# Kernel optimization log

Measured on AMD Instinct MI355X. Metric: run time of the kernel, lower is better.

The kernel has to match this reference:

```python
import math
import jax, jax.numpy as jnp
import numpy as np

D_MODEL = 1024
NUM_HEADS = 16
HEAD_DIM = D_MODEL // NUM_HEADS
CAUSAL = True


def setup_inputs() -> dict:
    key = jax.random.key(0)
    ks = jax.random.split(key, 9)
    B, S = 2, 2048
    s = 1.0 / math.sqrt(D_MODEL)
    x = jax.random.normal(ks[0], (B, S, D_MODEL), dtype=jnp.float32)
    Wq = jax.random.normal(ks[1], (D_MODEL, D_MODEL), dtype=jnp.float32) * s
    bq = jax.random.normal(ks[2], (D_MODEL,), dtype=jnp.float32) * 0.01
    Wk = jax.random.normal(ks[3], (D_MODEL, D_MODEL), dtype=jnp.float32) * s
    bk = jax.random.normal(ks[4], (D_MODEL,), dtype=jnp.float32) * 0.01
    Wv = jax.random.normal(ks[5], (D_MODEL, D_MODEL), dtype=jnp.float32) * s
    bv = jax.random.normal(ks[6], (D_MODEL,), dtype=jnp.float32) * 0.01
    Wo = jax.random.normal(ks[7], (D_MODEL, D_MODEL), dtype=jnp.float32) * s
    bo = jax.random.normal(ks[8], (D_MODEL,), dtype=jnp.float32) * 0.01
    return {"x": x, "Wq": Wq, "bq": bq, "Wk": Wk, "bk": bk,
            "Wv": Wv, "bv": bv, "Wo": Wo, "bo": bo}


def reference(x, Wq, bq, Wk, bk, Wv, bv, Wo, bo):
    B, S, _ = x.shape
    # projections (torch Linear: x @ W.T + b; here W already stored as [in,out])
    q = x @ Wq + bq
    k = x @ Wk + bk
    v = x @ Wv + bv
    # split heads -> [B, H, S, hd]
    def split(t):
        return t.reshape(B, S, NUM_HEADS, HEAD_DIM).transpose(0, 2, 1, 3)
    q, k, v = split(q), split(k), split(v)
    scores = jnp.einsum('bhqd,bhkd->bhqk', q, k) / math.sqrt(HEAD_DIM)
    if CAUSAL:
        causal = jnp.tril(jnp.ones((S, S), dtype=bool))  # True = keep
        scores = jnp.where(causal, scores, -jnp.inf)
    attn = jax.nn.softmax(scores, axis=-1)
    out = jnp.einsum('bhqk,bhkd->bhqd', attn, v)
    out = out.transpose(0, 2, 1, 3).reshape(B, S, D_MODEL)
    return out @ Wo + bo
```

## Files before the change

### kernel.cpp

```cpp
#include <hip/hip_runtime.h>
#include <hip/hip_bf16.h>

typedef __bf16 bf16_t;
typedef __bf16 v8bf __attribute__((ext_vector_type(8)));
typedef float  v4f  __attribute__((ext_vector_type(4)));

#define MFMA16(a, b, c) __builtin_amdgcn_mfma_f32_16x16x32_bf16((a), (b), (c), 0, 0, 0)

#define GLDS16(g, l) __builtin_amdgcn_global_load_lds(                         \
    (const __attribute__((address_space(1))) void*)(g),                        \
    (__attribute__((address_space(3))) void*)(l), 16, 0, 0)

#define VMEMCNT(n) asm volatile("s_waitcnt vmcnt(" #n ")" ::: "memory")
#define SBAR()     __builtin_amdgcn_s_barrier()
#define SFENCE()   __builtin_amdgcn_sched_barrier(0)

#define B_SZ   2
#define SEQ    2048
#define DM     1024
#define NH     16
#define HD     64
#define M_TOT  4096

#define QSCALE 0.18033688011112043f

__global__ __launch_bounds__(256)
void conv_x_kernel(const float* __restrict__ src, bf16_t* __restrict__ dst)
{
    int i = (blockIdx.x * 256 + threadIdx.x) * 8;
    float4 a = *reinterpret_cast<const float4*>(src + i);
    float4 b = *reinterpret_cast<const float4*>(src + i + 4);
    union { bf16_t h[8]; int4 v; } u;
    u.h[0] = (bf16_t)a.x; u.h[1] = (bf16_t)a.y; u.h[2] = (bf16_t)a.z; u.h[3] = (bf16_t)a.w;
    u.h[4] = (bf16_t)b.x; u.h[5] = (bf16_t)b.y; u.h[6] = (bf16_t)b.z; u.h[7] = (bf16_t)b.w;
    *reinterpret_cast<int4*>(dst + i) = u.v;
}

__global__ __launch_bounds__(256)
void conv_wt_kernel(const float* __restrict__ Wq, const float* __restrict__ Wk,
                    const float* __restrict__ Wv, const float* __restrict__ Wo,
                    bf16_t* __restrict__ WqkvT, bf16_t* __restrict__ WoT)
{
    __shared__ float t[32][33];
    const int z = blockIdx.z;
    const float* src = (z == 0) ? Wq : (z == 1) ? Wk : (z == 2) ? Wv : Wo;
    bf16_t* dst = (z < 3) ? (WqkvT + (size_t)z * 1048576) : WoT;
    const int tx = threadIdx.x & 31, ty = threadIdx.x >> 5;
    const int c0 = blockIdx.x * 32, r0 = blockIdx.y * 32;
#pragma unroll
    for (int i = 0; i < 4; ++i)
        t[ty + i * 8][tx] = src[(size_t)(r0 + ty + i * 8) * DM + c0 + tx];
    __syncthreads();
#pragma unroll
    for (int i = 0; i < 4; ++i)
        dst[(size_t)(c0 + ty + i * 8) * DM + r0 + tx] = (bf16_t)t[tx][ty + i * 8];
}

__global__ __launch_bounds__(256)
void gemm_qkv_kernel(const bf16_t* __restrict__ A, const bf16_t* __restrict__ BT,
                     const float* __restrict__ b0, const float* __restrict__ b1,
                     const float* __restrict__ b2,
                     bf16_t* __restrict__ oQ, bf16_t* __restrict__ oK,
                     bf16_t* __restrict__ oV)
{
    __shared__ __align__(16) bf16_t As[2 * 128 * 64];
    __shared__ __align__(16) bf16_t Bs[2 * 192 * 64];

    const int tid  = threadIdx.x;
    const int lane = tid & 63;
    const int wave = tid >> 6;
    const int wm   = (wave >> 1) * 64;
    const int wn   = (wave & 1) * 96;
    const int quad = lane >> 4;
    const int l15  = lane & 15;
    const int l7   = l15 & 7;

    const int n0 = blockIdx.x * 192;
    const int m0 = blockIdx.y * 128;

    const bf16_t *ap[4], *bp[6];
#pragma unroll
    for (int i = 0; i < 4; ++i) {
        int cidx = (wave * 4 + i) * 64 + lane;
        int r = cidx >> 3;
        int c = (cidx & 7) ^ (r & 7);
        ap[i] = A + (size_t)(m0 + r) * DM + c * 8;
    }
#pragma unroll
    for (int i = 0; i < 6; ++i) {
        int cidx = (wave * 6 + i) * 64 + lane;
        int r = cidx >> 3;
        int c = (cidx & 7) ^ (r & 7);
        bp[i] = BT + (size_t)(n0 + r) * DM + c * 8;
    }

    const v4f vzero = {0.f, 0.f, 0.f, 0.f};
    v4f acc[4][6];
#pragma unroll
    for (int mt = 0; mt < 4; ++mt)
#pragma unroll
        for (int nt = 0; nt < 6; ++nt) acc[mt][nt] = vzero;

#pragma unroll
    for (int i = 0; i < 4; ++i) { GLDS16(ap[i], As + (wave * 4 + i) * 512); ap[i] += 64; }
#pragma unroll
    for (int i = 0; i < 6; ++i) { GLDS16(bp[i], Bs + (wave * 6 + i) * 512); bp[i] += 64; }
#pragma unroll
    for (int i = 0; i < 4; ++i) { GLDS16(ap[i], As + 8192 + (wave * 4 + i) * 512); ap[i] += 64; }
#pragma unroll
    for (int i = 0; i < 6; ++i) { GLDS16(bp[i], Bs + 12288 + (wave * 6 + i) * 512); bp[i] += 64; }

    for (int it = 0; it < 16; ++it) {
        const int cur = it & 1;
        if (it < 15) { VMEMCNT(10); } else { VMEMCNT(0); }
        SBAR(); SFENCE();
#pragma unroll
        for (int ks = 0; ks < 2; ++ks) {
            v8bf af[4], bfq[6];
#pragma unroll
            for (int mt = 0; mt < 4; ++mt)
                af[mt] = *reinterpret_cast<const v8bf*>(
                    &As[cur * 8192 + (wm + mt * 16 + l15) * 64 + ((ks * 4 + quad) ^ l7) * 8]);
#pragma unroll
            for (int nt = 0; nt < 6; ++nt)
                bfq[nt] = *reinterpret_cast<const v8bf*>(
                    &Bs[cur * 12288 + (wn + nt * 16 + l15) * 64 + ((ks * 4 + quad) ^ l7) * 8]);
#pragma unroll
            for (int mt = 0; mt < 4; ++mt)
#pragma unroll
                for (int nt = 0; nt < 6; ++nt)
                    acc[mt][nt] = MFMA16(bfq[nt], af[mt], acc[mt][nt]);
        }
        SFENCE(); SBAR();
        if (it < 14) {
#pragma unroll
            for (int i = 0; i < 4; ++i) {
                GLDS16(ap[i], As + cur * 8192 + (wave * 4 + i) * 512);
                ap[i] += 64;
            }
#pragma unroll
            for (int i = 0; i < 6; ++i) {
                GLDS16(bp[i], Bs + cur * 12288 + (wave * 6 + i) * 512);
                bp[i] += 64;
            }
        }
    }

#pragma unroll
    for (int nt = 0; nt < 6; ++nt) {
        const int cf0 = n0 + wn + nt * 16;
        const int mat = cf0 >> 10;
        const int cw  = cf0 & 1023;
        if (mat != 2) {
            bf16_t* dst = (mat == 0) ? oQ : oK;
            const float scale = (mat == 0) ? QSCALE : 1.0f;
            const float* bias = (mat == 0) ? b0 : b1;
            const int h = cw >> 6;
            const int dbase = (cw & 63) + quad * 4;
            float4 bv = *reinterpret_cast<const float4*>(bias + cw + quad * 4);
#pragma unroll
            for (int mt = 0; mt < 4; ++mt) {
                int srow = m0 + wm + mt * 16 + l15;
                int b = srow >> 11, s = srow & 2047;
                union { bf16_t hh[4]; int2 v; } u;
                u.hh[0] = (bf16_t)((acc[mt][nt][0] + bv.x) * scale);
                u.hh[1] = (bf16_t)((acc[mt][nt][1] + bv.y) * scale);
                u.hh[2] = (bf16_t)((acc[mt][nt][2] + bv.z) * scale);
                u.hh[3] = (bf16_t)((acc[mt][nt][3] + bv.w) * scale);
                *reinterpret_cast<int2*>(
                    dst + ((size_t)(b * NH + h) * SEQ + s) * HD + dbase) = u.v;
            }
        } else {
#pragma unroll
            for (int r = 0; r < 4; ++r) {
                int cwe = cw + quad * 4 + r;
                float bvv = b2[cwe];
                int h = cwe >> 6, d = cwe & 63;
#pragma unroll
                for (int mt = 0; mt < 4; ++mt) {
                    int srow = m0 + wm + mt * 16 + l15;
                    int b = srow >> 11, s = srow & 2047;
                    oV[((size_t)(b * NH + h) * HD + d) * SEQ + s] =
                        (bf16_t)(acc[mt][nt][r] + bvv);
                }
            }
        }
    }
}

__global__ __launch_bounds__(256)
void gemm_o_kernel(const bf16_t* __restrict__ A, const bf16_t* __restrict__ BT,
                   const float* __restrict__ bias, float* __restrict__ out)
{
    __shared__ __align__(16) bf16_t As[2 * 128 * 64];
    __shared__ __align__(16) bf16_t Bs[2 * 64 * 64];

    const int tid  = threadIdx.x;
    const int lane = tid & 63;
    const int wave = tid >> 6;
    const int wm   = (wave >> 1) * 64;
    const int wn   = (wave & 1) * 32;
    const int quad = lane >> 4;
    const int l15  = lane & 15;
    const int l7   = l15 & 7;

    const int n0 = blockIdx.x * 64;
    const int m0 = blockIdx.y * 128;

    const bf16_t *ap[4], *bp[2];
#pragma unroll
    for (int i = 0; i < 4; ++i) {
        int cidx = (wave * 4 + i) * 64 + lane;
        int r = cidx >> 3;
        int c = (cidx & 7) ^ (r & 7);
        ap[i] = A + (size_t)(m0 + r) * DM + c * 8;
    }
#pragma unroll
    for (int i = 0; i < 2; ++i) {
        int cidx = (wave * 2 + i) * 64 + lane;
        int r = cidx >> 3;
        int c = (cidx & 7) ^ (r & 7);
        bp[i] = BT + (size_t)(n0 + r) * DM + c * 8;
    }

    const v4f vzero = {0.f, 0.f, 0.f, 0.f};
    v4f acc[4][2];
#pragma unroll
    for (int mt = 0; mt < 4; ++mt)
#pragma unroll
        for (int nt = 0; nt < 2; ++nt) acc[mt][nt] = vzero;

#pragma unroll
    for (int i = 0; i < 4; ++i) { GLDS16(ap[i], As + (wave * 4 + i) * 512); ap[i] += 64; }
#pragma unroll
    for (int i = 0; i < 2; ++i) { GLDS16(bp[i], Bs + (wave * 2 + i) * 512); bp[i] += 64; }
#pragma unroll
    for (int i = 0; i < 4; ++i) { GLDS16(ap[i], As + 8192 + (wave * 4 + i) * 512); ap[i] += 64; }
#pragma unroll
    for (int i = 0; i < 2; ++i) { GLDS16(bp[i], Bs + 4096 + (wave * 2 + i) * 512); bp[i] += 64; }

    for (int it = 0; it < 16; ++it) {
        const int cur = it & 1;
        if (it < 15) { VMEMCNT(6); } else { VMEMCNT(0); }
        SBAR(); SFENCE();
#pragma unroll
        for (int ks = 0; ks < 2; ++ks) {
            v8bf af[4], bfq[2];
#pragma unroll
            for (int mt = 0; mt < 4; ++mt)
                af[mt] = *reinterpret_cast<const v8bf*>(
                    &As[cur * 8192 + (wm + mt * 16 + l15) * 64 + ((ks * 4 + quad) ^ l7) * 8]);
#pragma unroll
            for (int nt = 0; nt < 2; ++nt)
                bfq[nt] = *reinterpret_cast<const v8bf*>(
                    &Bs[cur * 4096 + (wn + nt * 16 + l15) * 64 + ((ks * 4 + quad) ^ l7) * 8]);
#pragma unroll
            for (int mt = 0; mt < 4; ++mt)
#pragma unroll
                for (int nt = 0; nt < 2; ++nt)
                    acc[mt][nt] = MFMA16(af[mt], bfq[nt], acc[mt][nt]);
        }
        SFENCE(); SBAR();
        if (it < 14) {
#pragma unroll
            for (int i = 0; i < 4; ++i) {
                GLDS16(ap[i], As + cur * 8192 + (wave * 4 + i) * 512);
                ap[i] += 64;
            }
#pragma unroll
            for (int i = 0; i < 2; ++i) {
                GLDS16(bp[i], Bs + cur * 4096 + (wave * 2 + i) * 512);
                bp[i] += 64;
            }
        }
    }

#pragma unroll
    for (int mt = 0; mt < 4; ++mt) {
#pragma unroll
        for (int nt = 0; nt < 2; ++nt) {
            int col = n0 + wn + nt * 16 + l15;
            float bv = bias[col];
#pragma unroll
            for (int r = 0; r < 4; ++r) {
                int row = m0 + wm + mt * 16 + quad * 4 + r;
                out[(size_t)row * DM + col] = acc[mt][nt][r] + bv;
            }
        }
    }
}

__global__ __launch_bounds__(256)
void attn_kernel(const bf16_t* __restrict__ Q, const bf16_t* __restrict__ K,
                 const bf16_t* __restrict__ Vt, bf16_t* __restrict__ O)
{
    __shared__ __align__(16) bf16_t Ks[3][64 * 64];
    __shared__ __align__(16) bf16_t Vs[3][64 * 64];
    __shared__ float Ored[4 * 1040];
    __shared__ float lred[4 * 64];

    const int tid  = threadIdx.x;
    const int lane = tid & 63;
    const int w    = tid >> 6;
    const int quad = lane >> 4;
    const int l15  = lane & 15;
    const int l7   = lane & 7;

    const int bid = blockIdx.x;
    const int xcd = bid & 7;
    const int j   = bid >> 3;
    const int bh  = (xcd << 2) | (j >> 4);
    const int p   = j & 15;
    const size_t base = (size_t)bh * SEQ * HD;
    const bf16_t* Qg = Q  + base;
    const bf16_t* Kg = K  + base;
    const bf16_t* Vg = Vt + base;

    const int rr0 = tid >> 3;
    const int cc0 = (tid & 7) ^ (rr0 & 7);
    const int bO = bh >> 4, hO = bh & 15;
    const v4f vzero = {0.f, 0.f, 0.f, 0.f};

    for (int phase = 0; phase < 2; ++phase) {
        const int t  = phase ? (31 - p) : p;
        const int q0 = t * 64;

        v8bf qf[4][2];
#pragma unroll
        for (int g = 0; g < 4; ++g) {
            const bf16_t* qrow = Qg + (size_t)(q0 + g * 16 + l15) * HD;
            qf[g][0] = *reinterpret_cast<const v8bf*>(qrow + quad * 8);
            qf[g][1] = *reinterpret_cast<const v8bf*>(qrow + 32 + quad * 8);
        }

        const bf16_t* kp0 = Kg + (size_t)rr0 * HD + cc0 * 8;
        const bf16_t* kp1 = kp0 + 32 * HD;
        const bf16_t* vp0 = Vg + (size_t)rr0 * SEQ + cc0 * 8;
        const bf16_t* vp1 = vp0 + (size_t)32 * SEQ;

        v4f acc_p[4][4];
#pragma unroll
        for (int dt = 0; dt < 4; ++dt)
#pragma unroll
            for (int g = 0; g < 4; ++g) acc_p[dt][g] = vzero;
        float lp[4] = {0.f, 0.f, 0.f, 0.f};

        VMEMCNT(0);
        SBAR();
        GLDS16(kp0, &Ks[0][w * 512]);
        GLDS16(kp1, &Ks[0][2048 + w * 512]);
        GLDS16(vp0, &Vs[0][w * 512]);
        GLDS16(vp1, &Vs[0][2048 + w * 512]);
        kp0 += 64 * HD;  kp1 += 64 * HD;  vp0 += 64;  vp1 += 64;
        if (t >= 1) {
            GLDS16(kp0, &Ks[1][w * 512]);
            GLDS16(kp1, &Ks[1][2048 + w * 512]);
            GLDS16(vp0, &Vs[1][w * 512]);
            GLDS16(vp1, &Vs[1][2048 + w * 512]);
            kp0 += 64 * HD;  kp1 += 64 * HD;  vp0 += 64;  vp1 += 64;
        }
        if (t >= 2) {
            GLDS16(kp0, &Ks[2][w * 512]);
            GLDS16(kp1, &Ks[2][2048 + w * 512]);
            GLDS16(vp0, &Vs[2][w * 512]);
            GLDS16(vp1, &Vs[2][2048 + w * 512]);
            kp0 += 64 * HD;  kp1 += 64 * HD;  vp0 += 64;  vp1 += 64;
        }

        int cur = 0;
        for (int kt = 0; kt <= t; ++kt) {
            if (kt + 2 <= t)      { VMEMCNT(8); }
            else if (kt + 1 <= t) { VMEMCNT(4); }
            else                  { VMEMCNT(0); }
            SBAR(); SFENCE();

            v4f st[4];
#pragma unroll
            for (int g = 0; g < 4; ++g) st[g] = vzero;
#pragma unroll
            for (int ks = 0; ks < 2; ++ks) {
                v8bf kf = *reinterpret_cast<const v8bf*>(
                    &Ks[cur][(16 * w + l15) * 64 + ((ks * 4 + quad) ^ l7) * 8]);
#pragma unroll
                for (int g = 0; g < 4; ++g)
                    st[g] = MFMA16(kf, qf[g][ks], st[g]);
            }

            const bool diagI = (kt == t);
            v8bf pa[4];
#pragma unroll
            for (int g = 0; g < 4; ++g) {
                union { bf16_t h[8]; v8bf v; } up;
                up.h[4] = (bf16_t)0.f; up.h[5] = (bf16_t)0.f;
                up.h[6] = (bf16_t)0.f; up.h[7] = (bf16_t)0.f;
                if (diagI && g < w) {
                    up.h[0] = (bf16_t)0.f; up.h[1] = (bf16_t)0.f;
                    up.h[2] = (bf16_t)0.f; up.h[3] = (bf16_t)0.f;
                } else if (diagI && g == w) {
#pragma unroll
                    for (int r = 0; r < 4; ++r) {
                        float pv = (quad * 4 + r > l15)
                                     ? 0.f : __builtin_amdgcn_exp2f(st[g][r]);
                        lp[g] += pv;
                        up.h[r] = (bf16_t)pv;
                    }
                } else {
#pragma unroll
                    for (int r = 0; r < 4; ++r) {
                        float pv = __builtin_amdgcn_exp2f(st[g][r]);
                        lp[g] += pv;
                        up.h[r] = (bf16_t)pv;
                    }
                }
                pa[g] = up.v;
            }

#pragma unroll
            for (int dt = 0; dt < 4; ++dt) {
                const int rowd = dt * 16 + l15;
                uint2 vv = *reinterpret_cast<const uint2*>(
                    &Vs[cur][rowd * 64 +
                             (((2 * w + (quad >> 1)) ^ l7) * 8 + (quad & 1) * 4)]);
                union { unsigned u[4]; v8bf v; } uv;
                uv.u[0] = vv.x; uv.u[1] = vv.y; uv.u[2] = 0u; uv.u[3] = 0u;
#pragma unroll
                for (int g = 0; g < 4; ++g)
                    acc_p[dt][g] = MFMA16(uv.v, pa[g], acc_p[dt][g]);
            }

            SFENCE(); SBAR();
            if (kt + 3 <= t) {
                GLDS16(kp0, &Ks[cur][w * 512]);
                GLDS16(kp1, &Ks[cur][2048 + w * 512]);
                GLDS16(vp0, &Vs[cur][w * 512]);
                GLDS16(vp1, &Vs[cur][2048 + w * 512]);
                kp0 += 64 * HD;  kp1 += 64 * HD;  vp0 += 64;  vp1 += 64;
            }
            cur = (cur == 2) ? 0 : cur + 1;
        }

#pragma unroll
        for (int g = 0; g < 4; ++g) {
            lp[g] += __shfl_xor(lp[g], 16);
            lp[g] += __shfl_xor(lp[g], 32);
        }
        if (quad == 0) {
#pragma unroll
            for (int g = 0; g < 4; ++g)
                lred[w * 64 + g * 16 + l15] = lp[g];
        }

        const int qq = tid >> 2;
        const int db = (tid & 3) * 4;
        float linv = 0.f;
#pragma unroll
        for (int dt = 0; dt < 4; ++dt) {
#pragma unroll
            for (int g = 0; g < 4; ++g)
#pragma unroll
                for (int r = 0; r < 4; ++r)
                    Ored[w * 1040 + (quad * 4 + r) * 65 + g * 16 + l15] =
                        acc_p[dt][g][r];
            SBAR();
            if (dt == 0)
                linv = 1.f / (lred[qq] + lred[64 + qq] +
                              lred[128 + qq] + lred[192 + qq]);
            union { bf16_t h[4]; int2 v; } u;
#pragma unroll
            for (int e = 0; e < 4; ++e) {
                float s = Ored[(db + e) * 65 + qq]
                        + Ored[1040 + (db + e) * 65 + qq]
                        + Ored[2080 + (db + e) * 65 + qq]
                        + Ored[3120 + (db + e) * 65 + qq];
                u.h[e] = (bf16_t)(s * linv);
            }
            *reinterpret_cast<int2*>(
                &O[((size_t)bO * SEQ + q0 + qq) * DM + hO * 64 + dt * 16 + db]) = u.v;
            SBAR();
        }
    }
}

extern "C" void kernel_launch(void* const* d_in, const int* in_sizes, int n_in,
                              void* d_out, int out_size, void* d_ws, size_t ws_size,
                              hipStream_t stream) {
    const float* x  = (const float*)d_in[0];
    const float* Wq = (const float*)d_in[1];
    const float* bq = (const float*)d_in[2];
    const float* Wk = (const float*)d_in[3];
    const float* bk = (const float*)d_in[4];
    const float* Wv = (const float*)d_in[5];
    const float* bv = (const float*)d_in[6];
    const float* Wo = (const float*)d_in[7];
    const float* bo = (const float*)d_in[8];

    bf16_t* ws = (bf16_t*)d_ws;
    bf16_t* xb     = ws;
    bf16_t* WqkvT  = ws + 4194304;
    bf16_t* WoT    = ws + 7340032;
    bf16_t* Qb     = ws + 8388608;
    bf16_t* Kb     = ws + 12582912;
    bf16_t* Vb     = ws + 16777216;
    bf16_t* Ob     = ws;

    conv_x_kernel<<<2048, 256, 0, stream>>>(x, xb);
    conv_wt_kernel<<<dim3(32, 32, 4), 256, 0, stream>>>(Wq, Wk, Wv, Wo, WqkvT, WoT);
    gemm_qkv_kernel<<<dim3(16, 32), 256, 0, stream>>>(xb, WqkvT, bq, bk, bv, Qb, Kb, Vb);
    attn_kernel<<<512, 256, 0, stream>>>(Qb, Kb, Vb, Ob);
    gemm_o_kernel<<<dim3(16, 32), 256, 0, stream>>>(Ob, WoT, bo, (float*)d_out);
}
```

Before: 179.1 us.

## Process two KV tiles per iteration to fill the PV MFMA K dimension

The attention loop now handles a pair of 64-key tiles per iteration, using four LDS stages. Each PV MFMA packs the probabilities and V values of both tiles into the 32-wide K dimension, where before half of that operand was zero padding. This halves the PV MFMA count and the number of barriers per key. The price is that for even diagonal tiles an extra, fully masked KV tile is loaded and its QK product is computed. The Ored and lred reduction buffers now alias the K/V staging LDS, so the larger pipeline fits in the same shared-memory budget.

```diff
diff --git a/kernel.cpp b/kernel.cpp
--- a/kernel.cpp
+++ b/kernel.cpp
@@ -294,10 +294,10 @@
 void attn_kernel(const bf16_t* __restrict__ Q, const bf16_t* __restrict__ K,
                  const bf16_t* __restrict__ Vt, bf16_t* __restrict__ O)
 {
-    __shared__ __align__(16) bf16_t Ks[3][64 * 64];
-    __shared__ __align__(16) bf16_t Vs[3][64 * 64];
-    __shared__ float Ored[4 * 1040];
-    __shared__ float lred[4 * 64];
+    __shared__ __align__(16) bf16_t Ks[4][64 * 64];
+    __shared__ __align__(16) bf16_t Vs[4][64 * 64];
+    float* Ored = reinterpret_cast<float*>(&Ks[0][0]);
+    float* lred = reinterpret_cast<float*>(&Vs[0][0]);
 
     const int tid  = threadIdx.x;
     const int lane = tid & 63;
@@ -324,6 +324,8 @@
     for (int phase = 0; phase < 2; ++phase) {
         const int t  = phase ? (31 - p) : p;
         const int q0 = t * 64;
+        const int ns = (t + 2) >> 1;
+        const bool tEven = ((t & 1) == 0);
 
         v8bf qf[4][2];
 #pragma unroll
@@ -347,96 +349,114 @@
 
         VMEMCNT(0);
         SBAR();
-        GLDS16(kp0, &Ks[0][w * 512]);
-        GLDS16(kp1, &Ks[0][2048 + w * 512]);
-        GLDS16(vp0, &Vs[0][w * 512]);
-        GLDS16(vp1, &Vs[0][2048 + w * 512]);
-        kp0 += 64 * HD;  kp1 += 64 * HD;  vp0 += 64;  vp1 += 64;
-        if (t >= 1) {
-            GLDS16(kp0, &Ks[1][w * 512]);
-            GLDS16(kp1, &Ks[1][2048 + w * 512]);
-            GLDS16(vp0, &Vs[1][w * 512]);
-            GLDS16(vp1, &Vs[1][2048 + w * 512]);
+
+#pragma unroll
+        for (int s = 0; s < 2; ++s) {
+            GLDS16(kp0, &Ks[s][w * 512]);  GLDS16(kp1, &Ks[s][2048 + w * 512]);
+            GLDS16(vp0, &Vs[s][w * 512]);  GLDS16(vp1, &Vs[s][2048 + w * 512]);
             kp0 += 64 * HD;  kp1 += 64 * HD;  vp0 += 64;  vp1 += 64;
         }
-        if (t >= 2) {
-            GLDS16(kp0, &Ks[2][w * 512]);
-            GLDS16(kp1, &Ks[2][2048 + w * 512]);
-            GLDS16(vp0, &Vs[2][w * 512]);
-            GLDS16(vp1, &Vs[2][2048 + w * 512]);
-            kp0 += 64 * HD;  kp1 += 64 * HD;  vp0 += 64;  vp1 += 64;
-        }
-
-        int cur = 0;
-        for (int kt = 0; kt <= t; ++kt) {
-            if (kt + 2 <= t)      { VMEMCNT(8); }
-            else if (kt + 1 <= t) { VMEMCNT(4); }
-            else                  { VMEMCNT(0); }
+        if (ns > 1) {
+#pragma unroll
+            for (int s = 2; s < 4; ++s) {
+                GLDS16(kp0, &Ks[s][w * 512]);  GLDS16(kp1, &Ks[s][2048 + w * 512]);
+                GLDS16(vp0, &Vs[s][w * 512]);  GLDS16(vp1, &Vs[s][2048 + w * 512]);
+                kp0 += 64 * HD;  kp1 += 64 * HD;  vp0 += 64;  vp1 += 64;
+            }
+        }
+
+        for (int si = 0; si < ns; ++si) {
+            const int sA = (si & 1) * 2, sB = sA + 1;
+            if (si + 1 < ns) { VMEMCNT(8); } else { VMEMCNT(0); }
             SBAR(); SFENCE();
 
-            v4f st[4];
-#pragma unroll
-            for (int g = 0; g < 4; ++g) st[g] = vzero;
+            const bool last  = (si == ns - 1);
+            const bool diagA = last && tEven;
+            const bool diagB = last && !tEven;
+
+            v4f stA[4], stB[4];
+#pragma unroll
+            for (int g = 0; g < 4; ++g) { stA[g] = vzero; stB[g] = vzero; }
 #pragma unroll
             for (int ks = 0; ks < 2; ++ks) {
-                v8bf kf = *reinterpret_cast<const v8bf*>(
-                    &Ks[cur][(16 * w + l15) * 64 + ((ks * 4 + quad) ^ l7) * 8]);
-#pragma unroll
-                for (int g = 0; g < 4; ++g)
-                    st[g] = MFMA16(kf, qf[g][ks], st[g]);
-            }
-
-            const bool diagI = (kt == t);
+                const int koff = (16 * w + l15) * 64 + ((ks * 4 + quad) ^ l7) * 8;
+                v8bf kfA = *reinterpret_cast<const v8bf*>(&Ks[sA][koff]);
+                v8bf kfB = *reinterpret_cast<const v8bf*>(&Ks[sB][koff]);
+#pragma unroll
+                for (int g = 0; g < 4; ++g) {
+                    stA[g] = MFMA16(kfA, qf[g][ks], stA[g]);
+                    stB[g] = MFMA16(kfB, qf[g][ks], stB[g]);
+                }
+            }
+
             v8bf pa[4];
 #pragma unroll
             for (int g = 0; g < 4; ++g) {
                 union { bf16_t h[8]; v8bf v; } up;
-                up.h[4] = (bf16_t)0.f; up.h[5] = (bf16_t)0.f;
-                up.h[6] = (bf16_t)0.f; up.h[7] = (bf16_t)0.f;
-                if (diagI && g < w) {
+                if (diagA && g < w) {
                     up.h[0] = (bf16_t)0.f; up.h[1] = (bf16_t)0.f;
                     up.h[2] = (bf16_t)0.f; up.h[3] = (bf16_t)0.f;
-                } else if (diagI && g == w) {
+                } else if (diagA && g == w) {
 #pragma unroll
                     for (int r = 0; r < 4; ++r) {
                         float pv = (quad * 4 + r > l15)
-                                     ? 0.f : __builtin_amdgcn_exp2f(st[g][r]);
+                                     ? 0.f : __builtin_amdgcn_exp2f(stA[g][r]);
                         lp[g] += pv;
                         up.h[r] = (bf16_t)pv;
                     }
                 } else {
 #pragma unroll
                     for (int r = 0; r < 4; ++r) {
-                        float pv = __builtin_amdgcn_exp2f(st[g][r]);
+                        float pv = __builtin_amdgcn_exp2f(stA[g][r]);
                         lp[g] += pv;
                         up.h[r] = (bf16_t)pv;
                     }
                 }
+                if (diagA || (diagB && g < w)) {
+                    up.h[4] = (bf16_t)0.f; up.h[5] = (bf16_t)0.f;
+                    up.h[6] = (bf16_t)0.f; up.h[7] = (bf16_t)0.f;
+                } else if (diagB && g == w) {
+#pragma unroll
+                    for (int r = 0; r < 4; ++r) {
+                        float pv = (quad * 4 + r > l15)
+                                     ? 0.f : __builtin_amdgcn_exp2f(stB[g][r]);
+                        lp[g] += pv;
+                        up.h[4 + r] = (bf16_t)pv;
+                    }
+                } else {
+#pragma unroll
+                    for (int r = 0; r < 4; ++r) {
+                        float pv = __builtin_amdgcn_exp2f(stB[g][r]);
+                        lp[g] += pv;
+                        up.h[4 + r] = (bf16_t)pv;
+                    }
+                }
                 pa[g] = up.v;
             }
 
 #pragma unroll
             for (int dt = 0; dt < 4; ++dt) {
                 const int rowd = dt * 16 + l15;
-                uint2 vv = *reinterpret_cast<const uint2*>(
-                    &Vs[cur][rowd * 64 +
-                             (((2 * w + (quad >> 1)) ^ l7) * 8 + (quad & 1) * 4)]);
+                const int voff = rowd * 64 +
+                    (((2 * w + (quad >> 1)) ^ l7) * 8 + (quad & 1) * 4);
+                uint2 va = *reinterpret_cast<const uint2*>(&Vs[sA][voff]);
+                uint2 vb = *reinterpret_cast<const uint2*>(&Vs[sB][voff]);
                 union { unsigned u[4]; v8bf v; } uv;
-                uv.u[0] = vv.x; uv.u[1] = vv.y; uv.u[2] = 0u; uv.u[3] = 0u;
+                uv.u[0] = va.x; uv.u[1] = va.y; uv.u[2] = vb.x; uv.u[3] = vb.y;
 #pragma unroll
                 for (int g = 0; g < 4; ++g)
                     acc_p[dt][g] = MFMA16(uv.v, pa[g], acc_p[dt][g]);
             }
 
             SFENCE(); SBAR();
-            if (kt + 3 <= t) {
-                GLDS16(kp0, &Ks[cur][w * 512]);
-                GLDS16(kp1, &Ks[cur][2048 + w * 512]);
-                GLDS16(vp0, &Vs[cur][w * 512]);
-                GLDS16(vp1, &Vs[cur][2048 + w * 512]);
+            if (si + 2 < ns) {
+                GLDS16(kp0, &Ks[sA][w * 512]);  GLDS16(kp1, &Ks[sA][2048 + w * 512]);
+                GLDS16(vp0, &Vs[sA][w * 512]);  GLDS16(vp1, &Vs[sA][2048 + w * 512]);
                 kp0 += 64 * HD;  kp1 += 64 * HD;  vp0 += 64;  vp1 += 64;
-            }
-            cur = (cur == 2) ? 0 : cur + 1;
+                GLDS16(kp0, &Ks[sB][w * 512]);  GLDS16(kp1, &Ks[sB][2048 + w * 512]);
+                GLDS16(vp0, &Vs[sB][w * 512]);  GLDS16(vp1, &Vs[sB][2048 + w * 512]);
+                kp0 += 64 * HD;  kp1 += 64 * HD;  vp0 += 64;  vp1 += 64;
+            }
         }
 
 #pragma unroll
```

Result: faster. 173.8 us, median of 2 (-2.9%).
